# Kernel optimization log

Measured on AMD Instinct MI355X. Metric: run time of the kernel, lower is better.

Reference implementation:

```python
import jax, jax.numpy as jnp
import numpy as np

L, D, HID, QH, KVH, V, B, S, R = 2, 1024, 4096, 16, 4, 32000, 2, 2048, 20
HEAD, G = D // QH, QH // KVH
ALPHA, THETA = 32.0, 50000.0


def setup_inputs() -> dict:
    key = jax.random.key(0)
    ks = iter(jax.random.split(key, 40))
    def w(shape, s=0.02):
        return jax.random.normal(next(ks), shape, jnp.float32) * s
    KD = KVH * HEAD
    return {
        'xs': jax.random.randint(next(ks), (B, S), 0, V, dtype=jnp.int32),
        'emb': w((V, D)),
        'Wq': w((L, D, D)), 'bq': w((L, D)),
        'Wk': w((L, D, KD)), 'bk': w((L, KD)),
        'Wv': w((L, D, KD)), 'bv': w((L, KD)),
        'Wo': w((L, D, D)), 'bo': w((L, D)),
        'att_scale': 1.0 + w((L, D)),
        'mlp_scale': 1.0 + w((L, D)),
        'final_scale': 1.0 + w((D,)),
        'W1': w((L, D, HID)), 'A1': w((L, D, R)), 'a1b': w((L, R)), 'B1': w((L, R, HID)), 'b1b': w((L, HID)),
        'W2': w((L, D, HID)), 'A2': w((L, D, R)), 'a2b': w((L, R)), 'B2': w((L, R, HID)), 'b2b': w((L, HID)),
        'W3': w((L, HID, D)), 'A3': w((L, HID, R)), 'a3b': w((L, R)), 'B3': w((L, R, D)), 'b3b': w((L, D)),
        'startpos': 0,
    }


def _rms(x, scale):
    return scale * x * jax.lax.rsqrt(jnp.mean(x * x, axis=-1, keepdims=True) + 1e-5)


def _lora(x, Wl, Aw, ab, Bw, bb):
    # base linear output is detached in the original (no grad through it)
    return jax.lax.stop_gradient(x @ Wl) + ((x @ Aw + ab) @ Bw + bb) / ALPHA


def _forward(xs, startpos, emb, Wq, bq, Wk, bk, Wv, bv, Wo, bo,
             att_scale, mlp_scale, final_scale,
             W1, A1, a1b, B1, b1b, W2, A2, a2b, B2, b2b, W3, A3, a3b, B3, b3b):
    x = emb[xs]  # (B,S,D)
    # RoPE tables (head dim = D//QH, pairs rotated as complex numbers)
    freqs = 1.0 / THETA ** (jnp.arange(0, HEAD, 2, dtype=jnp.float32) / HEAD)  # (HEAD//2,)
    pos = jnp.arange(startpos, startpos + S, dtype=jnp.float32)
    ang = pos[:, None] * freqs[None, :]  # (S, HEAD//2)
    cos, sin = jnp.cos(ang), jnp.sin(ang)

    def rope(t):  # t: (B,S,H,HEAD)
        tr = t.reshape(t.shape[:-1] + (HEAD // 2, 2))
        t0, t1 = tr[..., 0], tr[..., 1]
        c, s = cos[None, :, None, :], sin[None, :, None, :]
        return jnp.stack((t0 * c - t1 * s, t0 * s + t1 * c), axis=-1).reshape(t.shape)

    causal = jnp.arange(S)[None, :] <= jnp.arange(S)[:, None]  # (Sq, Skv)
    inv_sqrt_d = np.float32(1.0 / np.sqrt(HEAD))
    for l in range(L):
        h = _rms(x, att_scale[l])
        q = rope((h @ Wq[l] + bq[l]).reshape(B, S, QH, HEAD))
        k = rope((h @ Wk[l] + bk[l]).reshape(B, S, KVH, HEAD))
        v = (h @ Wv[l] + bv[l]).reshape(B, S, KVH, HEAD)
        # GQA: q heads grouped per kv head (q head i uses kv head i//G); no explicit KV repeat
        qg = q.reshape(B, S, KVH, G, HEAD)
        scores = jnp.einsum('bskgd,btkd->bkgst', qg, k) * inv_sqrt_d
        if startpos == 0:
            scores = jnp.where(causal[None, None, None], scores, -jnp.inf)
        attn = jax.nn.softmax(scores, axis=-1)
        o = jnp.einsum('bkgst,btkd->bskgd', attn, v).reshape(B, S, D)
        x = x + (o @ Wo[l] + bo[l])
        h2 = _rms(x, mlp_scale[l])
        m = _lora(h2, W1[l], A1[l], a1b[l], B1[l], b1b[l]) * jax.nn.silu(
            _lora(h2, W2[l], A2[l], a2b[l], B2[l], b2b[l]))
        x = x + _lora(m, W3[l], A3[l], a3b[l], B3[l], b3b[l])
    f = _rms(x, final_scale)
    return f @ emb.T  # tied logits (B,S,V)


def reference(xs, emb, Wq, bq, Wk, bk, Wv, bv, Wo, bo, att_scale, mlp_scale, final_scale,
              W1, A1, a1b, B1, b1b, W2, A2, a2b, B2, b2b, W3, A3, a3b, B3, b3b, startpos):
    return _forward(xs, startpos, emb, Wq, bq, Wk, bk, Wv, bv, Wo, bo,
                    att_scale, mlp_scale, final_scale,
                    W1, A1, a1b, B1, b1b, W2, A2, a2b, B2, b2b, W3, A3, a3b, B3, b3b)
```

## Files before the change

### kernel.cpp

```cpp
#include <hip/hip_runtime.h>
#include <hip/hip_bf16.h>
#include <math.h>

constexpr int L_   = 2;
constexpr int D_   = 1024;
constexpr int HID_ = 4096;
constexpr int QH_  = 16;
constexpr int KVH_ = 4;
constexpr int V_   = 32000;
constexpr int B_   = 2;
constexpr int S_   = 2048;
constexpr int R_   = 20;
constexpr int HEAD_ = D_ / QH_;
constexpr int KD_   = KVH_ * HEAD_;
constexpr int QKV_  = D_ + 2 * KD_;
constexpr int M_    = B_ * S_;
constexpr float INV_ALPHA_ = 1.0f / 32.0f;
constexpr float LOG_STEP_ = 0.3381180865f;

typedef unsigned short ushort_t;
typedef __attribute__((ext_vector_type(8))) short bf16x8;
typedef __attribute__((ext_vector_type(4))) float f32x4;
typedef __attribute__((address_space(1))) const unsigned int gas_u32;
typedef __attribute__((address_space(3))) unsigned int las_u32;

__device__ __forceinline__ void gload16(const void* g, void* l) {
  __builtin_amdgcn_global_load_lds((gas_u32*)g, (las_u32*)l, 16, 0, 0);
}

__device__ __forceinline__ ushort_t f2bf(float f) {
  union { float f; unsigned int u; } c; c.f = f;
  unsigned int u = c.u + 0x7FFFu + ((c.u >> 16) & 1u);
  return (ushort_t)(u >> 16);
}
__device__ __forceinline__ float bflo(unsigned int w) {
  union { unsigned int u; float f; } c; c.u = w << 16; return c.f;
}
__device__ __forceinline__ float bfhi(unsigned int w) {
  union { unsigned int u; float f; } c; c.u = w & 0xFFFF0000u; return c.f;
}

__global__ __launch_bounds__(256) void k_embed(const int* __restrict__ xs,
                                               const float* __restrict__ emb,
                                               float* __restrict__ x) {
  int i = blockIdx.x * blockDim.x + threadIdx.x;
  int total4 = M_ * D_ / 4;
  if (i >= total4) return;
  int row = i >> 8;
  int c4  = i & 255;
  const float4* src = reinterpret_cast<const float4*>(emb + (size_t)xs[row] * D_) + c4;
  reinterpret_cast<float4*>(x)[i] = *src;
}

__global__ __launch_bounds__(256) void k_rms(const float* __restrict__ x,
                                             const float* __restrict__ scale,
                                             ushort_t* __restrict__ out) {
  int row = blockIdx.x;
  const float* xr = x + (size_t)row * D_;
  float ss = 0.f;
  for (int i = threadIdx.x; i < D_; i += 256) { float v = xr[i]; ss += v * v; }
  for (int off = 32; off > 0; off >>= 1) ss += __shfl_down(ss, off);
  __shared__ float red[5];
  if ((threadIdx.x & 63) == 0) red[threadIdx.x >> 6] = ss;
  __syncthreads();
  if (threadIdx.x == 0)
    red[4] = rsqrtf((red[0] + red[1] + red[2] + red[3]) * (1.0f / D_) + 1e-5f);
  __syncthreads();
  float inv = red[4];
  ushort_t* orow = out + (size_t)row * D_;
  for (int i = threadIdx.x; i < D_; i += 256) orow[i] = f2bf(scale[i] * xr[i] * inv);
}

__global__ __launch_bounds__(256) void k_cast(const float* __restrict__ in,
                                              ushort_t* __restrict__ out, int n8) {
  int i = blockIdx.x * blockDim.x + threadIdx.x;
  if (i >= n8) return;
  const float4* p = reinterpret_cast<const float4*>(in) + i * 2;
  float4 a = p[0], b = p[1];
  ushort_t r[8] = { f2bf(a.x), f2bf(a.y), f2bf(a.z), f2bf(a.w),
                    f2bf(b.x), f2bf(b.y), f2bf(b.z), f2bf(b.w) };
  reinterpret_cast<uint4*>(out)[i] = *reinterpret_cast<uint4*>(r);
}

__global__ __launch_bounds__(256) void k_tcast(const float* __restrict__ in,
                                               ushort_t* __restrict__ out,
                                               int K, int N) {
  __shared__ float t[32][33];
  int n0 = blockIdx.x * 32, k0 = blockIdx.y * 32;
  int c = threadIdx.x & 31, r0 = threadIdx.x >> 5;
#pragma unroll
  for (int rr = 0; rr < 4; ++rr) {
    int r = r0 + rr * 8;
    t[r][c] = in[(size_t)(k0 + r) * N + n0 + c];
  }
  __syncthreads();
#pragma unroll
  for (int rr = 0; rr < 4; ++rr) {
    int r = r0 + rr * 8;
    out[(size_t)(n0 + r) * K + k0 + c] = f2bf(t[c][r]);
  }
}

__global__ __launch_bounds__(256) void k_qkvbias(const float* __restrict__ bq,
                                                 const float* __restrict__ bk,
                                                 const float* __restrict__ bv,
                                                 float* __restrict__ b) {
  int i = blockIdx.x * 256 + threadIdx.x;
  if (i >= QKV_) return;
  b[i] = i < D_ ? bq[i] : (i < D_ + KD_ ? bk[i - D_] : bv[i - D_ - KD_]);
}

__global__ __launch_bounds__(256) void k_ropeprep_k(const float* __restrict__ qkv,
                                                    ushort_t* __restrict__ Kb) {
  int i = blockIdx.x * 256 + threadIdx.x;
  int pi = i & 31;
  int kh = (i >> 5) & 3;
  int s  = (i >> 7) & (S_ - 1);
  int b  = i >> 18;
  float freq = expf(-LOG_STEP_ * (float)pi);
  float ang = (float)s * freq;
  float sn, cs;
  sincosf(ang, &sn, &cs);
  const float* p = qkv + (size_t)(b * S_ + s) * QKV_ + D_ + kh * 64 + 2 * pi;
  float t0 = p[0], t1 = p[1];
  ushort_t* q = Kb + (size_t)((b * KVH_ + kh) * S_ + s) * 64 + 2 * pi;
  q[0] = f2bf(t0 * cs - t1 * sn);
  q[1] = f2bf(t0 * sn + t1 * cs);
}

__global__ __launch_bounds__(256) void k_prep_v(const float* __restrict__ qkv,
                                                ushort_t* __restrict__ Vt) {
  __shared__ float t[32][33];
  int s0 = blockIdx.x * 32, d0 = blockIdx.y * 32, bkh = blockIdx.z;
  int c = threadIdx.x & 31, r0 = threadIdx.x >> 5;
#pragma unroll
  for (int rr = 0; rr < 4; ++rr) {
    int r = r0 + rr * 8;
    t[r][c] = qkv[(size_t)((bkh >> 2) * S_ + s0 + r) * QKV_ + D_ + KD_ + (bkh & 3) * 64 + d0 + c];
  }
  __syncthreads();
#pragma unroll
  for (int rr = 0; rr < 4; ++rr) {
    int r = r0 + rr * 8;
    Vt[(size_t)(bkh * 64 + d0 + r) * S_ + s0 + c] = f2bf(t[c][r]);
  }
}

__global__ __launch_bounds__(256) void k_attn3(const float* __restrict__ qkv,
                                               const ushort_t* __restrict__ Kb,
                                               const ushort_t* __restrict__ Vt,
                                               ushort_t* __restrict__ obf) {
  __shared__ ushort_t Ks[64 * 64];
  __shared__ ushort_t Vs[64 * 64];
  __shared__ ushort_t Ps[4][16 * 64];

  int bid = blockIdx.x;
  int qt = 31 - (bid & 31);
  int qh = (bid >> 5) & 15;
  int b  = bid >> 9;
  int kh = qh >> 2;
  int tid = threadIdx.x;
  int w = tid >> 6, lane = tid & 63;
  int q0 = qt * 64;

  const ushort_t* Kbh = Kb + (size_t)(b * KVH_ + kh) * S_ * 64;
  const ushort_t* Vth = Vt + (size_t)(b * KVH_ + kh) * 64 * S_;

  bf16x8 qa[2];
  {
    int pos = q0 + w * 16 + (lane & 15);
    const float* qp = qkv + (size_t)(b * S_ + pos) * QKV_ + qh * 64 + (lane >> 4) * 8;
#pragma unroll
    for (int kk = 0; kk < 2; ++kk) {
      float4 f0 = *reinterpret_cast<const float4*>(qp + kk * 32);
      float4 f1 = *reinterpret_cast<const float4*>(qp + kk * 32 + 4);
      float f[8] = {f0.x, f0.y, f0.z, f0.w, f1.x, f1.y, f1.z, f1.w};
      int dbase = (lane >> 4) * 8 + kk * 32;
      ushort_t tq[8];
#pragma unroll
      for (int p = 0; p < 4; ++p) {
        int pi = (dbase >> 1) + p;
        float freq = expf(-LOG_STEP_ * (float)pi);
        float ang = (float)pos * freq;
        float sn, cs;
        sincosf(ang, &sn, &cs);
        float t0 = f[2 * p], t1 = f[2 * p + 1];
        tq[2 * p]     = f2bf((t0 * cs - t1 * sn) * 0.125f);
        tq[2 * p + 1] = f2bf((t0 * sn + t1 * cs) * 0.125f);
      }
      qa[kk] = *reinterpret_cast<const bf16x8*>(tq);
    }
  }

  f32x4 oacc[4];
#pragma unroll
  for (int j = 0; j < 4; ++j) oacc[j] = {0.f, 0.f, 0.f, 0.f};
  float m[4] = {-1e30f, -1e30f, -1e30f, -1e30f};
  float l[4] = {0.f, 0.f, 0.f, 0.f};

  const int srow = lane >> 3;
  const int soff = ((lane & 7) ^ srow) * 16;

  for (int t0 = 0; t0 <= q0; t0 += 64) {
#pragma unroll
    for (int r = 0; r < 2; ++r) {
      int c = w * 2 + r;
      const char* gk = (const char*)Kbh + (size_t)(t0 + c * 8 + srow) * 128 + soff;
      gload16(gk, (char*)Ks + c * 1024);
      const char* gv = (const char*)Vth + (size_t)(c * 8 + srow) * (S_ * 2) + (size_t)t0 * 2 + soff;
      gload16(gv, (char*)Vs + c * 1024);
    }
    __syncthreads();

    f32x4 sacc[4];
#pragma unroll
    for (int j = 0; j < 4; ++j) sacc[j] = {0.f, 0.f, 0.f, 0.f};
#pragma unroll
    for (int kk = 0; kk < 2; ++kk) {
#pragma unroll
      for (int j = 0; j < 4; ++j) {
        int krow = j * 16 + (lane & 15);
        int chunk = kk * 4 + (lane >> 4);
        bf16x8 kf = *reinterpret_cast<const bf16x8*>(
            &Ks[krow * 64 + ((chunk ^ (krow & 7)) << 3)]);
        sacc[j] = __builtin_amdgcn_mfma_f32_16x16x32_bf16(qa[kk], kf, sacc[j], 0, 0, 0);
      }
    }
    if (t0 == q0) {
#pragma unroll
      for (int j = 0; j < 4; ++j)
#pragma unroll
        for (int e = 0; e < 4; ++e) {
          int keyr = j * 16 + (lane & 15);
          int qr = w * 16 + (lane >> 4) * 4 + e;
          if (keyr > qr) sacc[j][e] = -1e30f;
        }
    }

    float corr[4];
#pragma unroll
    for (int e = 0; e < 4; ++e) {
      float mt = fmaxf(fmaxf(sacc[0][e], sacc[1][e]), fmaxf(sacc[2][e], sacc[3][e]));
#pragma unroll
      for (int off = 1; off < 16; off <<= 1) mt = fmaxf(mt, __shfl_xor(mt, off));
      float mn = fmaxf(m[e], mt);
      corr[e] = __expf(m[e] - mn);
      m[e] = mn;
    }
    float rs[4] = {0.f, 0.f, 0.f, 0.f};
#pragma unroll
    for (int j = 0; j < 4; ++j)
#pragma unroll
      for (int e = 0; e < 4; ++e) {
        float p = __expf(sacc[j][e] - m[e]);
        sacc[j][e] = p;
        rs[e] += p;
      }
#pragma unroll
    for (int e = 0; e < 4; ++e) {
#pragma unroll
      for (int off = 1; off < 16; off <<= 1) rs[e] += __shfl_xor(rs[e], off);
      l[e] = l[e] * corr[e] + rs[e];
    }
#pragma unroll
    for (int j = 0; j < 4; ++j)
#pragma unroll
      for (int e = 0; e < 4; ++e) oacc[j][e] *= corr[e];

#pragma unroll
    for (int j = 0; j < 4; ++j)
#pragma unroll
      for (int e = 0; e < 4; ++e) {
        int prow = (lane >> 4) * 4 + e;
        int pcol = j * 16 + (lane & 15);
        Ps[w][prow * 64 + (((pcol >> 3) ^ (prow & 7)) << 3) + (pcol & 7)] = f2bf(sacc[j][e]);
      }

    bf16x8 pa[2];
    int prow2 = lane & 15;
#pragma unroll
    for (int kk = 0; kk < 2; ++kk) {
      int chunk = kk * 4 + (lane >> 4);
      pa[kk] = *reinterpret_cast<const bf16x8*>(
          &Ps[w][prow2 * 64 + ((chunk ^ (prow2 & 7)) << 3)]);
    }
#pragma unroll
    for (int kk = 0; kk < 2; ++kk) {
#pragma unroll
      for (int jd = 0; jd < 4; ++jd) {
        int vrow = jd * 16 + (lane & 15);
        int chunk = kk * 4 + (lane >> 4);
        bf16x8 vf = *reinterpret_cast<const bf16x8*>(
            &Vs[vrow * 64 + ((chunk ^ (vrow & 7)) << 3)]);
        oacc[jd] = __builtin_amdgcn_mfma_f32_16x16x32_bf16(pa[kk], vf, oacc[jd], 0, 0, 0);
      }
    }
    __syncthreads();
  }

#pragma unroll
  for (int e = 0; e < 4; ++e) {
    int tok = b * S_ + q0 + w * 16 + (lane >> 4) * 4 + e;
    float inv = 1.f / l[e];
#pragma unroll
    for (int jd = 0; jd < 4; ++jd) {
      int col = qh * 64 + jd * 16 + (lane & 15);
      obf[(size_t)tok * D_ + col] = f2bf(oacc[jd][e] * inv);
    }
  }
}

__global__ __launch_bounds__(256) void k_silumul(const ushort_t* __restrict__ g1,
                                                 const ushort_t* __restrict__ g2,
                                                 ushort_t* __restrict__ out) {
  int i = blockIdx.x * 256 + threadIdx.x;
  uint4 a4 = reinterpret_cast<const uint4*>(g1)[i];
  uint4 b4 = reinterpret_cast<const uint4*>(g2)[i];
  unsigned au[4] = {a4.x, a4.y, a4.z, a4.w};
  unsigned bu[4] = {b4.x, b4.y, b4.z, b4.w};
  ushort_t r[8];
#pragma unroll
  for (int q = 0; q < 4; ++q) {
    float a0 = bflo(au[q]), a1 = bfhi(au[q]);
    float b0 = bflo(bu[q]), b1 = bfhi(bu[q]);
    r[2 * q]     = f2bf(a0 * b0 / (1.f + __expf(-b0)));
    r[2 * q + 1] = f2bf(a1 * b1 / (1.f + __expf(-b1)));
  }
  reinterpret_cast<uint4*>(out)[i] = *reinterpret_cast<uint4*>(r);
}

__global__ __launch_bounds__(256) void k_trA(const float* __restrict__ A,
                                             ushort_t* __restrict__ At, int K) {
  int idx = blockIdx.x * 256 + threadIdx.x;
  if (idx >= K * R_) return;
  int k = idx / R_, r = idx - k * R_;
  At[(size_t)r * K + k] = f2bf(A[idx]);
}

template <int K>
__global__ __launch_bounds__(256) void k_loraA(const ushort_t* __restrict__ hbm,
                                               const ushort_t* __restrict__ At,
                                               const float* __restrict__ ab,
                                               float* __restrict__ u) {
  constexpr int E = K / 64;
  int row = blockIdx.x * 4 + (threadIdx.x >> 6);
  int lane = threadIdx.x & 63;
  float hf[E];
  {
    const uint4* hp = reinterpret_cast<const uint4*>(hbm + (size_t)row * K + lane * E);
#pragma unroll
    for (int i = 0; i < E / 8; ++i) {
      uint4 vv = hp[i];
      unsigned int wsv[4] = {vv.x, vv.y, vv.z, vv.w};
#pragma unroll
      for (int q = 0; q < 4; ++q) {
        hf[i * 8 + q * 2]     = bflo(wsv[q]);
        hf[i * 8 + q * 2 + 1] = bfhi(wsv[q]);
      }
    }
  }
  for (int r = 0; r < R_; ++r) {
    const uint4* ap = reinterpret_cast<const uint4*>(At + (size_t)r * K + lane * E);
    float acc = 0.f;
#pragma unroll
    for (int i = 0; i < E / 8; ++i) {
      uint4 av = ap[i];
      unsigned int wsv[4] = {av.x, av.y, av.z, av.w};
#pragma unroll
      for (int q = 0; q < 4; ++q) {
        acc = fmaf(hf[i * 8 + q * 2], bflo(wsv[q]), acc);
        acc = fmaf(hf[i * 8 + q * 2 + 1], bfhi(wsv[q]), acc);
      }
    }
#pragma unroll
    for (int off = 1; off < 64; off <<= 1) acc += __shfl_xor(acc, off);
    if (lane == 0) u[(size_t)row * R_ + r] = acc + ab[r];
  }
}

template <bool LORA, bool OBF>
__global__ __launch_bounds__(256) void k_bgemm(const ushort_t* __restrict__ A,
                                               const ushort_t* __restrict__ Bt,
                                               const float* __restrict__ bias,
                                               const float* __restrict__ u,
                                               const float* __restrict__ Bl,
                                               const float* __restrict__ lb,
                                               const float* __restrict__ Cin,
                                               void* __restrict__ Cout,
                                               int M, int N, int K) {
  __shared__ ushort_t lds[3][2][128 * 32];
  const int tid = threadIdx.x;
  const int lane = tid & 63;
  const int w = tid >> 6;
  const int wr = w >> 1, wc = w & 1;

  unsigned nwg = gridDim.x * gridDim.y;
  unsigned orig = blockIdx.y * gridDim.x + blockIdx.x;
  unsigned qq = nwg >> 3, r8 = nwg & 7;
  unsigned xcd = orig & 7, loc = orig >> 3;
  unsigned swz = (xcd < r8 ? xcd * (qq + 1) : r8 * (qq + 1) + (xcd - r8) * qq) + loc;
  const int bm = (int)(swz / gridDim.x) * 128;
  const int bn = (int)(swz % gridDim.x) * 128;

  f32x4 acc[4][4];
#pragma unroll
  for (int i = 0; i < 4; ++i)
#pragma unroll
    for (int j = 0; j < 4; ++j) acc[i][j] = {0.f, 0.f, 0.f, 0.f};

  const int srow = (lane >> 2);
  const int skcol = (lane & 3) * 8;
  const int nt = K >> 5;

#define STAGE_TILE(kt)                                                          \
  {                                                                             \
    int k0_ = (kt) * 32;                                                        \
    int sl_ = (kt) % 3;                                                         \
    _Pragma("unroll")                                                           \
    for (int q_ = 0; q_ < 2; ++q_) {                                            \
      int c_ = w * 2 + q_;                                                      \
      gload16(A + (size_t)(bm + c_ * 16 + srow) * K + k0_ + skcol,              \
              (char*)&lds[sl_][0][0] + c_ * 1024);                              \
      gload16(Bt + (size_t)(bn + c_ * 16 + srow) * K + k0_ + skcol,             \
              (char*)&lds[sl_][1][0] + c_ * 1024);                              \
    }                                                                           \
  }

  STAGE_TILE(0)
  STAGE_TILE(1)
  asm volatile("s_waitcnt vmcnt(4)\n\ts_barrier" ::: "memory");

  const int koff = (lane >> 4) * 8;
  const int rsel = lane & 15;

  for (int t = 0; t < nt; ++t) {
    if (t + 2 < nt) STAGE_TILE(t + 2)
    const ushort_t* As = &lds[t % 3][0][0];
    const ushort_t* Bs = &lds[t % 3][1][0];
    bf16x8 af[4], bfr[4];
#pragma unroll
    for (int i = 0; i < 4; ++i)
      af[i] = *reinterpret_cast<const bf16x8*>(&As[(wr * 64 + i * 16 + rsel) * 32 + koff]);
#pragma unroll
    for (int j = 0; j < 4; ++j)
      bfr[j] = *reinterpret_cast<const bf16x8*>(&Bs[(wc * 64 + j * 16 + rsel) * 32 + koff]);
    __builtin_amdgcn_s_setprio(1);
#pragma unroll
    for (int i = 0; i < 4; ++i)
#pragma unroll
      for (int j = 0; j < 4; ++j)
        acc[i][j] = __builtin_amdgcn_mfma_f32_16x16x32_bf16(af[i], bfr[j], acc[i][j], 0, 0, 0);
    __builtin_amdgcn_s_setprio(0);
    if (t + 2 < nt) {
      asm volatile("s_waitcnt vmcnt(4)\n\ts_barrier" ::: "memory");
    } else if (t + 1 < nt) {
      asm volatile("s_waitcnt vmcnt(0)\n\ts_barrier" ::: "memory");
    }
  }
#undef STAGE_TILE

  float* Cf = (float*)Cout;
  ushort_t* Cb = (ushort_t*)Cout;

  if constexpr (LORA) {
    asm volatile("s_barrier" ::: "memory");
    float* Us  = (float*)&lds[0][0][0];
    float* Bls = (float*)&lds[1][0][0];
    for (int t = tid; t < 128 * R_; t += 256) {
      Us[t] = u[(size_t)bm * R_ + t];
      int rr = t >> 7, nn = t & 127;
      Bls[t] = Bl[(size_t)rr * N + bn + nn];
    }
    __syncthreads();
#pragma unroll
    for (int i = 0; i < 4; ++i) {
      int rl0 = wr * 64 + i * 16 + (lane >> 4) * 4;
#pragma unroll
      for (int e = 0; e < 4; ++e) {
        int rl = rl0 + e;
        float u20[R_];
#pragma unroll
        for (int r = 0; r < R_; ++r) u20[r] = Us[rl * R_ + r];
#pragma unroll
        for (int j = 0; j < 4; ++j) {
          int cl = wc * 64 + j * 16 + (lane & 15);
          float ud = lb[bn + cl];
#pragma unroll
          for (int r = 0; r < R_; ++r) ud = fmaf(u20[r], Bls[r * 128 + cl], ud);
          int row = bm + rl, col = bn + cl;
          float vv = acc[i][j][e] + ud * INV_ALPHA_;
          if constexpr (OBF) {
            Cb[(size_t)row * N + col] = f2bf(vv);
          } else {
            if (Cin) vv += Cin[(size_t)row * N + col];
            Cf[(size_t)row * N + col] = vv;
          }
        }
      }
    }
  } else {
#pragma unroll
    for (int i = 0; i < 4; ++i) {
      int row0 = bm + wr * 64 + i * 16 + (lane >> 4) * 4;
#pragma unroll
      for (int j = 0; j < 4; ++j) {
        int col = bn + wc * 64 + j * 16 + (lane & 15);
        float bv = bias ? bias[col] : 0.f;
#pragma unroll
        for (int e = 0; e < 4; ++e) {
          int row = row0 + e;
          float vv = acc[i][j][e] + bv;
          if constexpr (OBF) {
            Cb[(size_t)row * N + col] = f2bf(vv);
          } else {
            if (Cin) vv += Cin[(size_t)row * N + col];
            Cf[(size_t)row * N + col] = vv;
          }
        }
      }
    }
  }
}

template <bool LORA, bool OBF>
__global__ __launch_bounds__(512, 2) void k_bgemm2(const ushort_t* __restrict__ A,
                                                   const ushort_t* __restrict__ Bt,
                                                   const float* __restrict__ bias,
                                                   const float* __restrict__ u,
                                                   const float* __restrict__ Bl,
                                                   const float* __restrict__ lb,
                                                   const float* __restrict__ Cin,
                                                   void* __restrict__ Cout,
                                                   int M, int N, int K) {
  __shared__ ushort_t lds[3][24576];
  const int tid = threadIdx.x;
  const int lane = tid & 63;
  const int w = tid >> 6;
  const int wr = w >> 1;
  const int wc = w & 1;

  unsigned nwg = gridDim.x * gridDim.y;
  unsigned orig = blockIdx.y * gridDim.x + blockIdx.x;
  unsigned qq = nwg >> 3, r8 = nwg & 7;
  unsigned xcd = orig & 7, loc = orig >> 3;
  unsigned swz = (xcd < r8 ? xcd * (qq + 1) : r8 * (qq + 1) + (xcd - r8) * qq) + loc;
  const int bm = (int)(swz / gridDim.x) * 256;
  const int bn = (int)(swz % gridDim.x) * 128;

  f32x4 acc[4][4];
#pragma unroll
  for (int i = 0; i < 4; ++i)
#pragma unroll
    for (int j = 0; j < 4; ++j) acc[i][j] = {0.f, 0.f, 0.f, 0.f};

  const int srow8 = lane >> 3;
  const int scol  = ((lane & 7) ^ srow8) * 8;
  const int nt = K >> 6;

#define STAGE2(kt)                                                              \
  {                                                                             \
    int k0_ = (kt) << 6;                                                        \
    int sl_ = (kt) % 3;                                                         \
    _Pragma("unroll")                                                           \
    for (int c_ = 0; c_ < 4; ++c_) {                                            \
      int ch = w * 4 + c_;                                                      \
      gload16(A + (size_t)(bm + ch * 8 + srow8) * K + k0_ + scol,               \
              (char*)&lds[sl_][0] + ch * 1024);                                 \
    }                                                                           \
    _Pragma("unroll")                                                           \
    for (int c_ = 0; c_ < 2; ++c_) {                                            \
      int ch = w * 2 + c_;                                                      \
      gload16(Bt + (size_t)(bn + ch * 8 + srow8) * K + k0_ + scol,              \
              (char*)&lds[sl_][16384] + ch * 1024);                             \
    }                                                                           \
  }

  STAGE2(0)
  STAGE2(1)
  asm volatile("s_waitcnt vmcnt(6)\n\ts_barrier" ::: "memory");

  const int rsel = lane & 15;
  const int g4 = lane >> 4;

  for (int t = 0; t < nt; ++t) {
    if (t + 2 < nt) STAGE2(t + 2)
    const ushort_t* As = &lds[t % 3][0];
    const ushort_t* Bs = &lds[t % 3][16384];
#pragma unroll
    for (int kk = 0; kk < 2; ++kk) {
      int slotA = kk * 4 + g4;
      bf16x8 af[4], bfr[4];
#pragma unroll
      for (int fm = 0; fm < 4; ++fm) {
        int row = wr * 64 + fm * 16 + rsel;
        af[fm] = *reinterpret_cast<const bf16x8*>(&As[row * 64 + ((slotA ^ (row & 7)) << 3)]);
      }
#pragma unroll
      for (int fn = 0; fn < 4; ++fn) {
        int row = wc * 64 + fn * 16 + rsel;
        bfr[fn] = *reinterpret_cast<const bf16x8*>(&Bs[row * 64 + ((slotA ^ (row & 7)) << 3)]);
      }
      __builtin_amdgcn_s_setprio(1);
#pragma unroll
      for (int fm = 0; fm < 4; ++fm)
#pragma unroll
        for (int fn = 0; fn < 4; ++fn)
          acc[fm][fn] = __builtin_amdgcn_mfma_f32_16x16x32_bf16(af[fm], bfr[fn], acc[fm][fn], 0, 0, 0);
      __builtin_amdgcn_s_setprio(0);
    }
    if (t + 2 < nt) {
      asm volatile("s_waitcnt vmcnt(6)\n\ts_barrier" ::: "memory");
    } else if (t + 1 < nt) {
      asm volatile("s_waitcnt vmcnt(0)\n\ts_barrier" ::: "memory");
    }
  }
#undef STAGE2

  float* Cf = (float*)Cout;
  ushort_t* Cb = (ushort_t*)Cout;

  if constexpr (LORA) {
    asm volatile("s_barrier" ::: "memory");
    float* Us  = (float*)&lds[0][0];
    float* Bls = (float*)&lds[1][0];
    for (int t2 = tid; t2 < 256 * R_; t2 += 512) Us[t2] = u[(size_t)bm * R_ + t2];
    for (int t2 = tid; t2 < R_ * 128; t2 += 512) {
      int rr = t2 >> 7, nn = t2 & 127;
      Bls[t2] = Bl[(size_t)rr * N + bn + nn];
    }
    __syncthreads();
#pragma unroll
    for (int fm = 0; fm < 4; ++fm) {
      int rl0 = wr * 64 + fm * 16 + g4 * 4;
#pragma unroll
      for (int e = 0; e < 4; ++e) {
        int rl = rl0 + e;
        float u20[R_];
#pragma unroll
        for (int r = 0; r < R_; ++r) u20[r] = Us[rl * R_ + r];
#pragma unroll
        for (int fn = 0; fn < 4; ++fn) {
          int cl = wc * 64 + fn * 16 + rsel;
          float ud = lb[bn + cl];
#pragma unroll
          for (int r = 0; r < R_; ++r) ud = fmaf(u20[r], Bls[r * 128 + cl], ud);
          int row = bm + rl, col = bn + cl;
          float vv = acc[fm][fn][e] + ud * INV_ALPHA_;
          if constexpr (OBF) {
            Cb[(size_t)row * N + col] = f2bf(vv);
          } else {
            if (Cin) vv += Cin[(size_t)row * N + col];
            Cf[(size_t)row * N + col] = vv;
          }
        }
      }
    }
  } else {
#pragma unroll
    for (int fm = 0; fm < 4; ++fm) {
      int row0 = bm + wr * 64 + fm * 16 + g4 * 4;
#pragma unroll
      for (int fn = 0; fn < 4; ++fn) {
        int col = bn + wc * 64 + fn * 16 + rsel;
        float bv = bias ? bias[col] : 0.f;
#pragma unroll
        for (int e = 0; e < 4; ++e) {
          int row = row0 + e;
          float vv = acc[fm][fn][e] + bv;
          if constexpr (OBF) {
            Cb[(size_t)row * N + col] = f2bf(vv);
          } else {
            if (Cin) vv += Cin[(size_t)row * N + col];
            Cf[(size_t)row * N + col] = vv;
          }
        }
      }
    }
  }
}

static inline void bgemm(hipStream_t st, const ushort_t* A, const ushort_t* Bt,
                         const float* bias, const float* Cin, float* C,
                         int M, int N, int K) {
  dim3 g(N / 128, M / 128);
  k_bgemm<false, false><<<g, 256, 0, st>>>(A, Bt, bias, nullptr, nullptr, nullptr, Cin, C, M, N, K);
}
static inline void bgemm_lora_f32(hipStream_t st, const ushort_t* A, const ushort_t* Bt,
                                  const float* u, const float* Bl, const float* lb,
                                  const float* Cin, float* C, int M, int N, int K) {
  dim3 g(N / 128, M / 128);
  k_bgemm<true, false><<<g, 256, 0, st>>>(A, Bt, nullptr, u, Bl, lb, Cin, C, M, N, K);
}
static inline void bgemm2(hipStream_t st, const ushort_t* A, const ushort_t* Bt,
                          const float* bias, const float* Cin, float* C,
                          int M, int N, int K) {
  dim3 g(N / 128, M / 256);
  k_bgemm2<false, false><<<g, 512, 0, st>>>(A, Bt, bias, nullptr, nullptr, nullptr, Cin, C, M, N, K);
}
static inline void bgemm2_lora_bf(hipStream_t st, const ushort_t* A, const ushort_t* Bt,
                                  const float* u, const float* Bl, const float* lb,
                                  ushort_t* C, int M, int N, int K) {
  dim3 g(N / 128, M / 256);
  k_bgemm2<true, true><<<g, 512, 0, st>>>(A, Bt, nullptr, u, Bl, lb, nullptr, C, M, N, K);
}
static inline void tcast(hipStream_t st, const float* in, ushort_t* out, int K, int N) {
  dim3 g(N / 32, K / 32);
  k_tcast<<<g, 256, 0, st>>>(in, out, K, N);
}

extern "C" void kernel_launch(void* const* d_in, const int* in_sizes, int n_in,
                              void* d_out, int out_size, void* d_ws, size_t ws_size,
                              hipStream_t stream) {
  (void)in_sizes; (void)n_in; (void)out_size; (void)ws_size;
  const int*   xs  = (const int*)d_in[0];
  const float* emb = (const float*)d_in[1];
  const float* Wq  = (const float*)d_in[2];
  const float* bq  = (const float*)d_in[3];
  const float* Wk  = (const float*)d_in[4];
  const float* bk  = (const float*)d_in[5];
  const float* Wv  = (const float*)d_in[6];
  const float* bv  = (const float*)d_in[7];
  const float* Wo  = (const float*)d_in[8];
  const float* bo  = (const float*)d_in[9];
  const float* att_scale   = (const float*)d_in[10];
  const float* mlp_scale   = (const float*)d_in[11];
  const float* final_scale = (const float*)d_in[12];
  const float* W1  = (const float*)d_in[13];
  const float* A1  = (const float*)d_in[14];
  const float* a1b = (const float*)d_in[15];
  const float* B1  = (const float*)d_in[16];
  const float* b1b = (const float*)d_in[17];
  const float* W2  = (const float*)d_in[18];
  const float* A2  = (const float*)d_in[19];
  const float* a2b = (const float*)d_in[20];
  const float* B2  = (const float*)d_in[21];
  const float* b2b = (const float*)d_in[22];
  const float* W3  = (const float*)d_in[23];
  const float* A3  = (const float*)d_in[24];
  const float* a3b = (const float*)d_in[25];
  const float* B3  = (const float*)d_in[26];
  const float* b3b = (const float*)d_in[27];
  float* out = (float*)d_out;

  float* ws   = (float*)d_ws;
  float* xbuf = ws;
  float* qkv  = xbuf + (size_t)M_ * D_;
  float* ubuf = qkv + (size_t)M_ * QKV_;
  float* qkvb = ubuf + (size_t)M_ * R_;
  ushort_t* g1b = (ushort_t*)(qkvb + QKV_);
  ushort_t* g2b = g1b + (size_t)M_ * HID_;
  ushort_t* hb  = g2b + (size_t)M_ * HID_;
  ushort_t* wT  = hb + (size_t)M_ * HID_;
  ushort_t* At  = wT + (size_t)HID_ * D_;
  ushort_t* embT = At + (size_t)R_ * HID_;
  ushort_t* Kb = g1b;
  ushort_t* Vt = Kb + (size_t)B_ * KVH_ * S_ * 64;

  k_embed<<<dim3(M_ * D_ / 4 / 256), dim3(256), 0, stream>>>(xs, emb, xbuf);

  for (int l = 0; l < L_; ++l) {
    k_rms<<<dim3(M_), dim3(256), 0, stream>>>(xbuf, att_scale + (size_t)l * D_, hb);
    tcast(stream, Wq + (size_t)l * D_ * D_, wT, D_, D_);
    tcast(stream, Wk + (size_t)l * D_ * KD_, wT + (size_t)D_ * D_, D_, KD_);
    tcast(stream, Wv + (size_t)l * D_ * KD_, wT + (size_t)(D_ + KD_) * D_, D_, KD_);
    k_qkvbias<<<dim3(6), dim3(256), 0, stream>>>(bq + (size_t)l * D_, bk + (size_t)l * KD_,
                                                 bv + (size_t)l * KD_, qkvb);
    bgemm(stream, hb, wT, qkvb, nullptr, qkv, M_, QKV_, D_);
    {
      int npk = M_ * KVH_ * 32;
      k_ropeprep_k<<<dim3(npk / 256), dim3(256), 0, stream>>>(qkv, Kb);
    }
    k_prep_v<<<dim3(S_ / 32, 2, B_ * KVH_), dim3(256), 0, stream>>>(qkv, Vt);
    k_attn3<<<dim3(B_ * QH_ * (S_ / 64)), dim3(256), 0, stream>>>(qkv, Kb, Vt, hb);
    tcast(stream, Wo + (size_t)l * D_ * D_, wT, D_, D_);
    bgemm(stream, hb, wT, bo + (size_t)l * D_, xbuf, xbuf, M_, D_, D_);

    k_rms<<<dim3(M_), dim3(256), 0, stream>>>(xbuf, mlp_scale + (size_t)l * D_, hb);
    k_trA<<<dim3((D_ * R_ + 255) / 256), dim3(256), 0, stream>>>(A1 + (size_t)l * D_ * R_, At, D_);
    k_loraA<D_><<<dim3(M_ / 4), dim3(256), 0, stream>>>(hb, At, a1b + (size_t)l * R_, ubuf);
    tcast(stream, W1 + (size_t)l * D_ * HID_, wT, D_, HID_);
    bgemm2_lora_bf(stream, hb, wT, ubuf, B1 + (size_t)l * R_ * HID_, b1b + (size_t)l * HID_,
                   g1b, M_, HID_, D_);
    k_trA<<<dim3((D_ * R_ + 255) / 256), dim3(256), 0, stream>>>(A2 + (size_t)l * D_ * R_, At, D_);
    k_loraA<D_><<<dim3(M_ / 4), dim3(256), 0, stream>>>(hb, At, a2b + (size_t)l * R_, ubuf);
    tcast(stream, W2 + (size_t)l * D_ * HID_, wT, D_, HID_);
    bgemm2_lora_bf(stream, hb, wT, ubuf, B2 + (size_t)l * R_ * HID_, b2b + (size_t)l * HID_,
                   g2b, M_, HID_, D_);
    k_silumul<<<dim3(M_ * HID_ / 8 / 256), dim3(256), 0, stream>>>(g1b, g2b, hb);
    k_trA<<<dim3((HID_ * R_ + 255) / 256), dim3(256), 0, stream>>>(A3 + (size_t)l * HID_ * R_, At, HID_);
    k_loraA<HID_><<<dim3(M_ / 4), dim3(256), 0, stream>>>(hb, At, a3b + (size_t)l * R_, ubuf);
    tcast(stream, W3 + (size_t)l * HID_ * D_, wT, HID_, D_);
    bgemm_lora_f32(stream, hb, wT, ubuf, B3 + (size_t)l * R_ * D_, b3b + (size_t)l * D_,
                   xbuf, xbuf, M_, D_, HID_);
  }

  k_rms<<<dim3(M_), dim3(256), 0, stream>>>(xbuf, final_scale, hb);
  {
    int n8 = (int)((size_t)V_ * D_ / 8);
    k_cast<<<dim3((n8 + 255) / 256), dim3(256), 0, stream>>>(emb, embT, n8);
  }
  bgemm2(stream, hb, embT, nullptr, nullptr, out, M_, V_, D_);
}
```

Before: 1.566 ms.

## Enlarge bf16 GEMM tile to 256x256 with double-buffered LDS staging

Replaces the 256x128 triple-buffered GEMM kernel with a 256x256 tile. Each of the 8 waves now computes a 128x64 sub-tile, and LDS staging drops to two buffers with the next load issued after a barrier at the end of each k-step. It is used for the LoRA W1/W2 projections and the tied-logit GEMM. The aim is more reuse per loaded byte and fewer workgroups, but the accumulator doubles to 128 registers under the (512,2) launch bound, which risks spills. The LDS footprint also rises to 128KB, and removing the third stage reduces load/compute overlap.

Result: faster. 1.491 ms (-4.8%).

```diff
diff --git a/kernel.cpp b/kernel.cpp
--- a/kernel.cpp
+++ b/kernel.cpp
@@ -523,7 +523,7 @@
 }
 
 template <bool LORA, bool OBF>
-__global__ __launch_bounds__(512, 2) void k_bgemm2(const ushort_t* __restrict__ A,
+__global__ __launch_bounds__(512, 2) void k_bgemm3(const ushort_t* __restrict__ A,
                                                    const ushort_t* __restrict__ Bt,
                                                    const float* __restrict__ bias,
                                                    const float* __restrict__ u,
@@ -532,12 +532,12 @@
                                                    const float* __restrict__ Cin,
                                                    void* __restrict__ Cout,
                                                    int M, int N, int K) {
-  __shared__ ushort_t lds[3][24576];
+  __shared__ ushort_t lds[2][32768];
   const int tid = threadIdx.x;
   const int lane = tid & 63;
   const int w = tid >> 6;
-  const int wr = w >> 1;
-  const int wc = w & 1;
+  const int wr = w >> 2;
+  const int wc = w & 3;
 
   unsigned nwg = gridDim.x * gridDim.y;
   unsigned orig = blockIdx.y * gridDim.x + blockIdx.x;
@@ -545,11 +545,11 @@
   unsigned xcd = orig & 7, loc = orig >> 3;
   unsigned swz = (xcd < r8 ? xcd * (qq + 1) : r8 * (qq + 1) + (xcd - r8) * qq) + loc;
   const int bm = (int)(swz / gridDim.x) * 256;
-  const int bn = (int)(swz % gridDim.x) * 128;
-
-  f32x4 acc[4][4];
-#pragma unroll
-  for (int i = 0; i < 4; ++i)
+  const int bn = (int)(swz % gridDim.x) * 256;
+
+  f32x4 acc[8][4];
+#pragma unroll
+  for (int i = 0; i < 8; ++i)
 #pragma unroll
     for (int j = 0; j < 4; ++j) acc[i][j] = {0.f, 0.f, 0.f, 0.f};
 
@@ -557,10 +557,10 @@
   const int scol  = ((lane & 7) ^ srow8) * 8;
   const int nt = K >> 6;
 
-#define STAGE2(kt)                                                              \
+#define STAGE3(kt)                                                              \
   {                                                                             \
     int k0_ = (kt) << 6;                                                        \
-    int sl_ = (kt) % 3;                                                         \
+    int sl_ = (kt) & 1;                                                         \
     _Pragma("unroll")                                                           \
     for (int c_ = 0; c_ < 4; ++c_) {                                            \
       int ch = w * 4 + c_;                                                      \
@@ -568,31 +568,30 @@
               (char*)&lds[sl_][0] + ch * 1024);                                 \
     }                                                                           \
     _Pragma("unroll")                                                           \
-    for (int c_ = 0; c_ < 2; ++c_) {                                            \
-      int ch = w * 2 + c_;                                                      \
+    for (int c_ = 0; c_ < 4; ++c_) {                                            \
+      int ch = w * 4 + c_;                                                      \
       gload16(Bt + (size_t)(bn + ch * 8 + srow8) * K + k0_ + scol,              \
               (char*)&lds[sl_][16384] + ch * 1024);                             \
     }                                                                           \
   }
 
-  STAGE2(0)
-  STAGE2(1)
-  asm volatile("s_waitcnt vmcnt(6)\n\ts_barrier" ::: "memory");
+  STAGE3(0)
+  STAGE3(1)
+  asm volatile("s_waitcnt vmcnt(8)\n\ts_barrier" ::: "memory");
 
   const int rsel = lane & 15;
   const int g4 = lane >> 4;
 
   for (int t = 0; t < nt; ++t) {
-    if (t + 2 < nt) STAGE2(t + 2)
-    const ushort_t* As = &lds[t % 3][0];
-    const ushort_t* Bs = &lds[t % 3][16384];
+    const ushort_t* As = &lds[t & 1][0];
+    const ushort_t* Bs = &lds[t & 1][16384];
 #pragma unroll
     for (int kk = 0; kk < 2; ++kk) {
       int slotA = kk * 4 + g4;
-      bf16x8 af[4], bfr[4];
-#pragma unroll
-      for (int fm = 0; fm < 4; ++fm) {
-        int row = wr * 64 + fm * 16 + rsel;
+      bf16x8 af[8], bfr[4];
+#pragma unroll
+      for (int fm = 0; fm < 8; ++fm) {
+        int row = wr * 128 + fm * 16 + rsel;
         af[fm] = *reinterpret_cast<const bf16x8*>(&As[row * 64 + ((slotA ^ (row & 7)) << 3)]);
       }
 #pragma unroll
@@ -602,19 +601,21 @@
       }
       __builtin_amdgcn_s_setprio(1);
 #pragma unroll
-      for (int fm = 0; fm < 4; ++fm)
+      for (int fm = 0; fm < 8; ++fm)
 #pragma unroll
         for (int fn = 0; fn < 4; ++fn)
           acc[fm][fn] = __builtin_amdgcn_mfma_f32_16x16x32_bf16(af[fm], bfr[fn], acc[fm][fn], 0, 0, 0);
       __builtin_amdgcn_s_setprio(0);
     }
+    asm volatile("s_barrier" ::: "memory");
     if (t + 2 < nt) {
-      asm volatile("s_waitcnt vmcnt(6)\n\ts_barrier" ::: "memory");
+      STAGE3(t + 2)
+      asm volatile("s_waitcnt vmcnt(8)\n\ts_barrier" ::: "memory");
     } else if (t + 1 < nt) {
       asm volatile("s_waitcnt vmcnt(0)\n\ts_barrier" ::: "memory");
     }
   }
-#undef STAGE2
+#undef STAGE3
 
   float* Cf = (float*)Cout;
   ushort_t* Cb = (ushort_t*)Cout;
@@ -624,14 +625,14 @@
     float* Us  = (float*)&lds[0][0];
     float* Bls = (float*)&lds[1][0];
     for (int t2 = tid; t2 < 256 * R_; t2 += 512) Us[t2] = u[(size_t)bm * R_ + t2];
-    for (int t2 = tid; t2 < R_ * 128; t2 += 512) {
-      int rr = t2 >> 7, nn = t2 & 127;
+    for (int t2 = tid; t2 < R_ * 256; t2 += 512) {
+      int rr = t2 >> 8, nn = t2 & 255;
       Bls[t2] = Bl[(size_t)rr * N + bn + nn];
     }
     __syncthreads();
 #pragma unroll
-    for (int fm = 0; fm < 4; ++fm) {
-      int rl0 = wr * 64 + fm * 16 + g4 * 4;
+    for (int fm = 0; fm < 8; ++fm) {
+      int rl0 = wr * 128 + fm * 16 + g4 * 4;
 #pragma unroll
       for (int e = 0; e < 4; ++e) {
         int rl = rl0 + e;
@@ -643,7 +644,7 @@
           int cl = wc * 64 + fn * 16 + rsel;
           float ud = lb[bn + cl];
 #pragma unroll
-          for (int r = 0; r < R_; ++r) ud = fmaf(u20[r], Bls[r * 128 + cl], ud);
+          for (int r = 0; r < R_; ++r) ud = fmaf(u20[r], Bls[r * 256 + cl], ud);
           int row = bm + rl, col = bn + cl;
           float vv = acc[fm][fn][e] + ud * INV_ALPHA_;
           if constexpr (OBF) {
@@ -657,8 +658,8 @@
     }
   } else {
 #pragma unroll
-    for (int fm = 0; fm < 4; ++fm) {
-      int row0 = bm + wr * 64 + fm * 16 + g4 * 4;
+    for (int fm = 0; fm < 8; ++fm) {
+      int row0 = bm + wr * 128 + fm * 16 + g4 * 4;
 #pragma unroll
       for (int fn = 0; fn < 4; ++fn) {
         int col = bn + wc * 64 + fn * 16 + rsel;
@@ -691,17 +692,17 @@
   dim3 g(N / 128, M / 128);
   k_bgemm<true, false><<<g, 256, 0, st>>>(A, Bt, nullptr, u, Bl, lb, Cin, C, M, N, K);
 }
-static inline void bgemm2(hipStream_t st, const ushort_t* A, const ushort_t* Bt,
+static inline void bgemm3(hipStream_t st, const ushort_t* A, const ushort_t* Bt,
                           const float* bias, const float* Cin, float* C,
                           int M, int N, int K) {
-  dim3 g(N / 128, M / 256);
-  k_bgemm2<false, false><<<g, 512, 0, st>>>(A, Bt, bias, nullptr, nullptr, nullptr, Cin, C, M, N, K);
-}
-static inline void bgemm2_lora_bf(hipStream_t st, const ushort_t* A, const ushort_t* Bt,
+  dim3 g(N / 256, M / 256);
+  k_bgemm3<false, false><<<g, 512, 0, st>>>(A, Bt, bias, nullptr, nullptr, nullptr, Cin, C, M, N, K);
+}
+static inline void bgemm3_lora_bf(hipStream_t st, const ushort_t* A, const ushort_t* Bt,
                                   const float* u, const float* Bl, const float* lb,
                                   ushort_t* C, int M, int N, int K) {
-  dim3 g(N / 128, M / 256);
-  k_bgemm2<true, true><<<g, 512, 0, st>>>(A, Bt, nullptr, u, Bl, lb, nullptr, C, M, N, K);
+  dim3 g(N / 256, M / 256);
+  k_bgemm3<true, true><<<g, 512, 0, st>>>(A, Bt, nullptr, u, Bl, lb, nullptr, C, M, N, K);
 }
 static inline void tcast(hipStream_t st, const float* in, ushort_t* out, int K, int N) {
   dim3 g(N / 32, K / 32);
@@ -779,12 +780,12 @@
     k_trA<<<dim3((D_ * R_ + 255) / 256), dim3(256), 0, stream>>>(A1 + (size_t)l * D_ * R_, At, D_);
     k_loraA<D_><<<dim3(M_ / 4), dim3(256), 0, stream>>>(hb, At, a1b + (size_t)l * R_, ubuf);
     tcast(stream, W1 + (size_t)l * D_ * HID_, wT, D_, HID_);
-    bgemm2_lora_bf(stream, hb, wT, ubuf, B1 + (size_t)l * R_ * HID_, b1b + (size_t)l * HID_,
+    bgemm3_lora_bf(stream, hb, wT, ubuf, B1 + (size_t)l * R_ * HID_, b1b + (size_t)l * HID_,
                    g1b, M_, HID_, D_);
     k_trA<<<dim3((D_ * R_ + 255) / 256), dim3(256), 0, stream>>>(A2 + (size_t)l * D_ * R_, At, D_);
     k_loraA<D_><<<dim3(M_ / 4), dim3(256), 0, stream>>>(hb, At, a2b + (size_t)l * R_, ubuf);
     tcast(stream, W2 + (size_t)l * D_ * HID_, wT, D_, HID_);
-    bgemm2_lora_bf(stream, hb, wT, ubuf, B2 + (size_t)l * R_ * HID_, b2b + (size_t)l * HID_,
+    bgemm3_lora_bf(stream, hb, wT, ubuf, B2 + (size_t)l * R_ * HID_, b2b + (size_t)l * HID_,
                    g2b, M_, HID_, D_);
     k_silumul<<<dim3(M_ * HID_ / 8 / 256), dim3(256), 0, stream>>>(g1b, g2b, hb);
     k_trA<<<dim3((HID_ * R_ + 255) / 256), dim3(256), 0, stream>>>(A3 + (size_t)l * HID_ * R_, At, HID_);
@@ -799,5 +800,5 @@
     int n8 = (int)((size_t)V_ * D_ / 8);
     k_cast<<<dim3((n8 + 255) / 256), dim3(256), 0, stream>>>(emb, embT, n8);
   }
-  bgemm2(stream, hb, embT, nullptr, nullptr, out, M_, V_, D_);
-}
+  bgemm3(stream, hb, embT, nullptr, nullptr, out, M_, V_, D_);
+}
```
